# Kernel tuning notes

Measured on AMD Instinct MI355X. Metric: run time of the kernel, lower is better.

The kernel has to match this reference:

```python
import jax, jax.numpy as jnp
import numpy as np

N, E, IN, OUT, R = 50000, 800000, 256, 256, 8
BN_EPS = 1e-5


def setup_inputs() -> dict:
    key = jax.random.key(0)
    ks = jax.random.split(key, 8)
    x = jax.random.normal(ks[0], (N, IN), dtype=jnp.float32)
    edge_index = jax.random.randint(ks[1], (2, E), 0, N, dtype=jnp.int64)
    # edge_attr: 5 float columns; column 4 carries the relation id in [0, R)
    edge_attr = jax.random.randint(ks[2], (E, 5), 0, R).astype(jnp.float32)
    # RGCNConv params (PyG defaults: root_weight=True, bias=True, aggr='mean')
    W = jax.random.normal(ks[3], (R, IN, OUT), dtype=jnp.float32) / np.sqrt(IN)
    root = jax.random.normal(ks[4], (IN, OUT), dtype=jnp.float32) / np.sqrt(IN)
    bias = jnp.zeros((OUT,), dtype=jnp.float32)
    # BatchNorm1d affine params
    gamma = jnp.ones((OUT,), dtype=jnp.float32)
    beta = jnp.zeros((OUT,), dtype=jnp.float32)
    # PReLU single shared slope (torch default init 0.25)
    prelu_a = jnp.asarray(0.25, dtype=jnp.float32)
    return {"x": x, "edge_index": edge_index, "edge_attr": edge_attr,
            "W": W, "root": root, "bias": bias,
            "gamma": gamma, "beta": beta, "prelu_a": prelu_a}


def _rgcn_block(x, edge_index, edge_type, W, root, bias, gamma, beta, prelu_a):
    src, dst = edge_index[0], edge_index[1]
    # per-(relation, dst) mean aggregation via a single segment_sum
    seg = edge_type.astype(jnp.int32) * N + dst.astype(jnp.int32)  # [E]
    msg_sum = jax.ops.segment_sum(x[src], seg, num_segments=R * N)  # [R*N, IN]
    cnt = jax.ops.segment_sum(jnp.ones((E,), x.dtype), seg, num_segments=R * N)
    mean = msg_sum.reshape(R, N, IN) / jnp.maximum(cnt, 1.0).reshape(R, N, 1)
    # relation-specific linear transforms, summed over relations, plus root + bias
    h = jnp.einsum('rni,rio->no', mean, W) + x @ root + bias  # [N, OUT]
    # BatchNorm1d (training mode: batch statistics over nodes)
    mu = jnp.mean(h, axis=0)
    var = jnp.mean(jnp.square(h - mu), axis=0)
    h = (h - mu) * jax.lax.rsqrt(var + BN_EPS) * gamma + beta
    # PReLU (single shared slope); dropout is identity at inference
    h = jnp.where(h > 0, h, prelu_a * h)
    # residual (in_channels == out_channels -> Identity projection)
    return h + x


def reference(x, edge_index, edge_attr, W, root, bias, gamma, beta, prelu_a):
    edge_type = edge_attr[:, 4].astype(jnp.int32)
    return _rgcn_block(x, edge_index, edge_type, W, root, bias, gamma, beta, prelu_a)
```

## Files before the change

kernel.cpp:

```cpp
#include <hip/hip_runtime.h>
#include <cstdio>
#include <cstdint>


constexpr int kN  = 50000;
constexpr int kE  = 800000;
constexpr int kR  = 8;
constexpr int kC  = 256;
constexpr int kMP = 50048;
constexpr int kK  = 2304;
constexpr int kWG = (kMP / 128) * (kC / 128);

typedef __attribute__((ext_vector_type(8))) short bf16x8;
typedef __attribute__((ext_vector_type(4))) float f32x4;
typedef __attribute__((ext_vector_type(2))) unsigned int u32x2;

__device__ __forceinline__ unsigned short f2bf(float f) {
  unsigned u = __builtin_bit_cast(unsigned, f);
  u = u + 0x7FFFu + ((u >> 16) & 1u);
  return (unsigned short)(u >> 16);
}
__device__ __forceinline__ float bf2f(unsigned short s) {
  unsigned u = ((unsigned)s) << 16;
  return __builtin_bit_cast(float, u);
}
__device__ __forceinline__ void gload16(const void* g, void* l) {
  __builtin_amdgcn_global_load_lds((__attribute__((address_space(1))) const void*)g,
                                   (__attribute__((address_space(3))) void*)l, 16, 0, 0);
}

__global__ void k_count(const int* __restrict__ ei, const float* __restrict__ ea,
                        int* __restrict__ cnt) {
  int e = blockIdx.x * blockDim.x + threadIdx.x;
  if (e >= kE) return;
  int dst = ei[kE + e];
  int rel = (int)ea[(size_t)e * 5 + 4];
  if ((unsigned)dst >= (unsigned)kN || (unsigned)rel >= (unsigned)kR) return;
  atomicAdd(&cnt[rel * kN + dst], 1);
}

__global__ void k_convert_x(const float* __restrict__ x, unsigned short* __restrict__ A) {
  int i = (blockIdx.x * blockDim.x + threadIdx.x) * 4;
  if (i >= kN * kC) return;
  int row = i >> 8, col = i & 255;
  float4 v = *(const float4*)(x + i);
  ushort4 o;
  o.x = f2bf(v.x); o.y = f2bf(v.y); o.z = f2bf(v.z); o.w = f2bf(v.w);
  *(ushort4*)(A + (size_t)row * kK + 2048 + col) = o;
}

__global__ void k_convert_w(const float* __restrict__ W, const float* __restrict__ root,
                            unsigned short* __restrict__ wbfT) {
  int t = blockIdx.x * blockDim.x + threadIdx.x;
  if (t >= kC * kK) return;
  int c = t / kK, k = t - c * kK;
  float v;
  if (k < kR * kC) {
    int r = k >> 8, kk = k & 255;
    v = W[(size_t)r * kC * kC + (size_t)kk * kC + c];
  } else {
    v = root[(size_t)(k - kR * kC) * kC + c];
  }
  wbfT[(size_t)c * kK + k] = f2bf(v);
}

__global__ void k_grp(const int* __restrict__ cnt, int* __restrict__ cursor,
                      int* __restrict__ gst, int* __restrict__ cur) {
  int t = blockIdx.x * blockDim.x + threadIdx.x;
  int lane = threadIdx.x & 63;
  int c[kR];
  int gsz = 0;
  if (t < kN) {
#pragma unroll
    for (int r = 0; r < kR; ++r) { c[r] = cnt[r * kN + t]; gsz += c[r]; }
  } else {
#pragma unroll
    for (int r = 0; r < kR; ++r) c[r] = 0;
  }
  int incl = gsz;
#pragma unroll
  for (int d = 1; d < 64; d <<= 1) {
    int v = __shfl_up(incl, d);
    if (lane >= d) incl += v;
  }
  int wtot = __shfl(incl, 63);
  int base = 0;
  if (lane == 63) base = atomicAdd(cursor, wtot);
  base = __shfl(base, 63);
  if (t < kN) {
    int o = base + incl - gsz;
#pragma unroll
    for (int r = 0; r < kR; ++r) { gst[r * kN + t] = o; cur[r * kN + t] = o; o += c[r]; }
  }
}

__global__ void k_fill(const int* __restrict__ ei, const float* __restrict__ ea,
                       int* __restrict__ cur, unsigned short* __restrict__ ebuf) {
  int e = blockIdx.x * blockDim.x + threadIdx.x;
  if (e >= kE) return;
  int src = ei[e];
  int dst = ei[kE + e];
  int rel = (int)ea[(size_t)e * 5 + 4];
  if ((unsigned)dst >= (unsigned)kN || (unsigned)rel >= (unsigned)kR) return;
  int pos = atomicAdd(&cur[rel * kN + dst], 1);
  ebuf[pos] = (unsigned short)src;
}

__global__ __launch_bounds__(256) void k_agg(const unsigned short* __restrict__ ebuf,
                                             const int* __restrict__ gst,
                                             const int* __restrict__ cnt,
                                             unsigned short* A) {
  int w = blockIdx.x * 4 + (threadIdx.x >> 6);
  int lane = threadIdx.x & 63;
  int r = w / kN, dst = w - r * kN;
  int st = gst[w], c = cnt[w];
  const unsigned short* xcols = A + 2048 + lane * 4;
  float s0 = 0.f, s1 = 0.f, s2 = 0.f, s3 = 0.f;
  for (int k = 0; k < c; ++k) {
    int src = ebuf[st + k];
    ushort4 v = *(const ushort4*)(xcols + (size_t)src * kK);
    s0 += bf2f(v.x); s1 += bf2f(v.y); s2 += bf2f(v.z); s3 += bf2f(v.w);
  }
  float sc = c > 0 ? 1.f / (float)c : 0.f;
  unsigned lo = (unsigned)f2bf(s0 * sc) | ((unsigned)f2bf(s1 * sc) << 16);
  unsigned hi = (unsigned)f2bf(s2 * sc) | ((unsigned)f2bf(s3 * sc) << 16);
  u32x2 pk = {lo, hi};
  __builtin_nontemporal_store(pk, (u32x2*)(A + (size_t)dst * kK + r * 256 + lane * 4));
}

__global__ __launch_bounds__(256) void k_gemm(const unsigned short* __restrict__ A,
                                              const unsigned short* __restrict__ wbfT,
                                              float* __restrict__ out,
                                              const float* __restrict__ bias,
                                              float* __restrict__ cs,
                                              float* __restrict__ csq) {
  __shared__ __align__(16) unsigned short As[128 * 64];
  __shared__ __align__(16) unsigned short Bs[128 * 64];
  const int tid = threadIdx.x;
  const int lane = tid & 63, wv = tid >> 6;
  const int bid = blockIdx.x;
  const int xcd = bid & 7, idx = bid >> 3;
  const int wgid = (xcd < 6 ? xcd * 98 : 588 + (xcd - 6) * 97) + idx;
  const int n0 = (wgid & 1) * 128, m0 = (wgid >> 1) * 128;
  const int wm = wv >> 1, wn = wv & 1;
  f32x4 acc[4][4] = {};

  constexpr int NT = kK / 64;
  for (int t = 0; t < NT; ++t) {
    const int kb = t * 64;
#pragma unroll
    for (int i = 0; i < 4; ++i) {
      int l = tid + 256 * i;
      int row = l >> 3;
      int sk = ((l & 7) ^ (row & 7)) * 8;
      gload16(A    + (size_t)(m0 + row) * kK + kb + sk, &As[l * 8]);
      gload16(wbfT + (size_t)(n0 + row) * kK + kb + sk, &Bs[l * 8]);
    }
    asm volatile("s_waitcnt vmcnt(0)" ::: "memory");
    __builtin_amdgcn_s_barrier();
    __builtin_amdgcn_sched_barrier(0);
#pragma unroll
    for (int kk = 0; kk < 64; kk += 32) {
      const int koff = kk + (lane >> 4) * 8;
      bf16x8 a[4], b[4];
#pragma unroll
      for (int i = 0; i < 4; ++i) {
        int ra = wm * 64 + i * 16 + (lane & 15);
        unsigned ba = (unsigned)(koff * 2) ^ (unsigned)((ra & 7) << 4);
        a[i] = *(const bf16x8*)((const char*)As + ra * 128 + ba);
        int rb = wn * 64 + i * 16 + (lane & 15);
        unsigned bb = (unsigned)(koff * 2) ^ (unsigned)((rb & 7) << 4);
        b[i] = *(const bf16x8*)((const char*)Bs + rb * 128 + bb);
      }
#pragma unroll
      for (int i = 0; i < 4; ++i)
#pragma unroll
        for (int j = 0; j < 4; ++j)
          acc[i][j] = __builtin_amdgcn_mfma_f32_16x16x32_bf16(a[i], b[j], acc[i][j], 0, 0, 0);
    }
    __builtin_amdgcn_s_barrier();
    __builtin_amdgcn_sched_barrier(0);
  }

#pragma unroll
  for (int j = 0; j < 4; ++j) {
    int col = n0 + wn * 64 + j * 16 + (lane & 15);
    float bv = bias[col];
    float s = 0.f, ss = 0.f;
#pragma unroll
    for (int i = 0; i < 4; ++i) {
      int rb = m0 + wm * 64 + i * 16 + (lane >> 4) * 4;
#pragma unroll
      for (int q = 0; q < 4; ++q) {
        float v = acc[i][j][q];
        s += v; ss += v * v;
        int row = rb + q;
        if (row < kN) out[(size_t)row * kC + col] = v + bv;
      }
    }
    s  += __shfl_xor(s, 16);  s  += __shfl_xor(s, 32);
    ss += __shfl_xor(ss, 16); ss += __shfl_xor(ss, 32);
    if (lane < 16) { atomicAdd(&cs[col], s); atomicAdd(&csq[col], ss); }
  }
}

__global__ void k_final(float* __restrict__ h, const float* __restrict__ x,
                        const float* __restrict__ cs, const float* __restrict__ csq,
                        const float* __restrict__ bias,
                        const float* __restrict__ gamma, const float* __restrict__ beta,
                        const float* __restrict__ prelu) {
  int idx = (blockIdx.x * blockDim.x + threadIdx.x) * 4;
  if (idx >= kN * kC) return;
  int col = idx & 255;
  const float inv_n = 1.0f / (float)kN;
  float a = prelu[0];
  float4 hv = *(float4*)(h + idx);
  float4 xv = *(const float4*)(x + idx);
  float hr[4] = {hv.x, hv.y, hv.z, hv.w};
  float xr[4] = {xv.x, xv.y, xv.z, xv.w};
#pragma unroll
  for (int j = 0; j < 4; ++j) {
    int c = col + j;
    float mu_raw = cs[c] * inv_n;
    float var = csq[c] * inv_n - mu_raw * mu_raw;
    float mu  = mu_raw + bias[c];
    float k   = gamma[c] * rsqrtf(var + 1e-5f);
    float v   = (hr[j] - mu) * k + beta[c];
    v = v > 0.f ? v : a * v;
    hr[j] = v + xr[j];
  }
  *(float4*)(h + idx) = make_float4(hr[0], hr[1], hr[2], hr[3]);
}

extern "C" void kernel_launch(void* const* d_in, const int* in_sizes, int n_in,
                              void* d_out, int out_size, void* d_ws, size_t ws_size,
                              hipStream_t stream) {
  const float* x     = (const float*)d_in[0];
  const int*   ei    = (const int*)d_in[1];
  const float* ea    = (const float*)d_in[2];
  const float* W     = (const float*)d_in[3];
  const float* root  = (const float*)d_in[4];
  const float* bias  = (const float*)d_in[5];
  const float* gamma = (const float*)d_in[6];
  const float* beta  = (const float*)d_in[7];
  const float* prelu = (const float*)d_in[8];
  float* out = (float*)d_out;
  char* ws = (char*)d_ws;

  size_t o = 0;
  auto alloc = [&](size_t sz) { size_t r = o; o += (sz + 255) & ~(size_t)255; return r; };
  size_t a_o    = alloc((size_t)kMP * kK * 2);
  size_t wbf_o  = alloc((size_t)kC * kK * 2);
  size_t cnt_o  = alloc((size_t)kR * kN * 4);
  size_t cs_o   = alloc(256 * 4);
  size_t csq_o  = alloc(256 * 4);
  size_t csr_o  = alloc(256);
  size_t zend   = o;
  size_t gst_o  = alloc((size_t)kR * kN * 4);
  size_t cur_o  = alloc((size_t)kR * kN * 4);
  size_t eb_o   = alloc((size_t)kE * 2);
  if (o > ws_size) {
    fprintf(stderr, "[RGCN kernel] ws too small: need %zu have %zu\n", o, ws_size);
    return;
  }

  unsigned short* A    = (unsigned short*)(ws + a_o);
  unsigned short* wbfT = (unsigned short*)(ws + wbf_o);
  int*   cnt    = (int*)(ws + cnt_o);
  float* cs     = (float*)(ws + cs_o);
  float* csq    = (float*)(ws + csq_o);
  int*   cursor = (int*)(ws + csr_o);
  int*   gst    = (int*)(ws + gst_o);
  int*   cur    = (int*)(ws + cur_o);
  unsigned short* ebuf = (unsigned short*)(ws + eb_o);

  hipMemsetAsync(ws + cnt_o, 0, zend - cnt_o, stream);
  hipMemsetAsync(ws + a_o + (size_t)kN * kK * 2, 0,
                 (size_t)(kMP - kN) * kK * 2, stream);
  k_count<<<(kE + 255) / 256, 256, 0, stream>>>(ei, ea, cnt);
  k_convert_x<<<(kN * kC / 4) / 256, 256, 0, stream>>>(x, A);
  k_convert_w<<<(kC * kK + 255) / 256, 256, 0, stream>>>(W, root, wbfT);
  k_grp<<<(kN + 255) / 256, 256, 0, stream>>>(cnt, cursor, gst, cur);
  k_fill<<<(kE + 255) / 256, 256, 0, stream>>>(ei, ea, cur, ebuf);
  k_agg<<<(kN * kR) / 4, 256, 0, stream>>>(ebuf, gst, cnt, A);
  k_gemm<<<kWG, 256, 0, stream>>>(A, wbfT, out, bias, cs, csq);
  k_final<<<(kN * kC / 4) / 256, 256, 0, stream>>>(out, x, cs, csq, bias, gamma, beta, prelu);
}
```

Before: 403.1 us.

## Fuse neighbor mean aggregation into GEMM, dropping the materialized A matrix

The separate aggregation kernel, which wrote a 50048x2304 bf16 concat matrix, and the tiled GEMM that re-read it are replaced by one fused kernel. Each 512-thread block gathers per-relation means for 64 destination nodes into LDS, then multiplies them against bf16 weights read directly from global memory, looping over 8 relations plus the root term. k_grp is reorganised so that, within each 64-node chunk, edges of one relation are laid out contiguously. This lets a wave walk one run of edges for 8 destinations at a time. It removes large HBM write and read traffic, but the GEMM now reads B from global or L2 without LDS staging, and the aggregation is serialised per wave inside the block.

```diff
diff --git a/kernel.cpp b/kernel.cpp
--- a/kernel.cpp
+++ b/kernel.cpp
@@ -7,9 +7,8 @@
 constexpr int kE  = 800000;
 constexpr int kR  = 8;
 constexpr int kC  = 256;
-constexpr int kMP = 50048;
 constexpr int kK  = 2304;
-constexpr int kWG = (kMP / 128) * (kC / 128);
+constexpr int kNB = 782;
 
 typedef __attribute__((ext_vector_type(8))) short bf16x8;
 typedef __attribute__((ext_vector_type(4))) float f32x4;
@@ -23,10 +22,6 @@
 __device__ __forceinline__ float bf2f(unsigned short s) {
   unsigned u = ((unsigned)s) << 16;
   return __builtin_bit_cast(float, u);
-}
-__device__ __forceinline__ void gload16(const void* g, void* l) {
-  __builtin_amdgcn_global_load_lds((__attribute__((address_space(1))) const void*)g,
-                                   (__attribute__((address_space(3))) void*)l, 16, 0, 0);
 }
 
 __global__ void k_count(const int* __restrict__ ei, const float* __restrict__ ea,
@@ -39,14 +34,13 @@
   atomicAdd(&cnt[rel * kN + dst], 1);
 }
 
-__global__ void k_convert_x(const float* __restrict__ x, unsigned short* __restrict__ A) {
+__global__ void k_convert_x(const float* __restrict__ x, unsigned short* __restrict__ xbf) {
   int i = (blockIdx.x * blockDim.x + threadIdx.x) * 4;
   if (i >= kN * kC) return;
-  int row = i >> 8, col = i & 255;
   float4 v = *(const float4*)(x + i);
   ushort4 o;
   o.x = f2bf(v.x); o.y = f2bf(v.y); o.z = f2bf(v.z); o.w = f2bf(v.w);
-  *(ushort4*)(A + (size_t)row * kK + 2048 + col) = o;
+  *(ushort4*)(xbf + i) = o;
 }
 
 __global__ void k_convert_w(const float* __restrict__ W, const float* __restrict__ root,
@@ -66,32 +60,23 @@
 
 __global__ void k_grp(const int* __restrict__ cnt, int* __restrict__ cursor,
                       int* __restrict__ gst, int* __restrict__ cur) {
-  int t = blockIdx.x * blockDim.x + threadIdx.x;
+  int wid = (blockIdx.x * blockDim.x + threadIdx.x) >> 6;
   int lane = threadIdx.x & 63;
-  int c[kR];
-  int gsz = 0;
-  if (t < kN) {
-#pragma unroll
-    for (int r = 0; r < kR; ++r) { c[r] = cnt[r * kN + t]; gsz += c[r]; }
-  } else {
-#pragma unroll
-    for (int r = 0; r < kR; ++r) c[r] = 0;
-  }
-  int incl = gsz;
-#pragma unroll
-  for (int d = 1; d < 64; d <<= 1) {
-    int v = __shfl_up(incl, d);
-    if (lane >= d) incl += v;
+  if (wid >= kR * kNB) return;
+  int r = wid / kNB, db = (wid - r * kNB) * 64;
+  int d = db + lane;
+  int c = (d < kN) ? cnt[r * kN + d] : 0;
+  int incl = c;
+#pragma unroll
+  for (int s = 1; s < 64; s <<= 1) {
+    int v = __shfl_up(incl, s);
+    if (lane >= s) incl += v;
   }
   int wtot = __shfl(incl, 63);
   int base = 0;
   if (lane == 63) base = atomicAdd(cursor, wtot);
   base = __shfl(base, 63);
-  if (t < kN) {
-    int o = base + incl - gsz;
-#pragma unroll
-    for (int r = 0; r < kR; ++r) { gst[r * kN + t] = o; cur[r * kN + t] = o; o += c[r]; }
-  }
+  if (d < kN) { int o = base + incl - c; gst[r * kN + d] = o; cur[r * kN + d] = o; }
 }
 
 __global__ void k_fill(const int* __restrict__ ei, const float* __restrict__ ea,
@@ -106,90 +91,133 @@
   ebuf[pos] = (unsigned short)src;
 }
 
-__global__ __launch_bounds__(256) void k_agg(const unsigned short* __restrict__ ebuf,
-                                             const int* __restrict__ gst,
-                                             const int* __restrict__ cnt,
-                                             unsigned short* A) {
-  int w = blockIdx.x * 4 + (threadIdx.x >> 6);
-  int lane = threadIdx.x & 63;
-  int r = w / kN, dst = w - r * kN;
-  int st = gst[w], c = cnt[w];
-  const unsigned short* xcols = A + 2048 + lane * 4;
-  float s0 = 0.f, s1 = 0.f, s2 = 0.f, s3 = 0.f;
-  for (int k = 0; k < c; ++k) {
-    int src = ebuf[st + k];
-    ushort4 v = *(const ushort4*)(xcols + (size_t)src * kK);
-    s0 += bf2f(v.x); s1 += bf2f(v.y); s2 += bf2f(v.z); s3 += bf2f(v.w);
-  }
-  float sc = c > 0 ? 1.f / (float)c : 0.f;
-  unsigned lo = (unsigned)f2bf(s0 * sc) | ((unsigned)f2bf(s1 * sc) << 16);
-  unsigned hi = (unsigned)f2bf(s2 * sc) | ((unsigned)f2bf(s3 * sc) << 16);
-  u32x2 pk = {lo, hi};
-  __builtin_nontemporal_store(pk, (u32x2*)(A + (size_t)dst * kK + r * 256 + lane * 4));
-}
-
-__global__ __launch_bounds__(256) void k_gemm(const unsigned short* __restrict__ A,
-                                              const unsigned short* __restrict__ wbfT,
-                                              float* __restrict__ out,
-                                              const float* __restrict__ bias,
-                                              float* __restrict__ cs,
-                                              float* __restrict__ csq) {
-  __shared__ __align__(16) unsigned short As[128 * 64];
-  __shared__ __align__(16) unsigned short Bs[128 * 64];
-  const int tid = threadIdx.x;
-  const int lane = tid & 63, wv = tid >> 6;
-  const int bid = blockIdx.x;
-  const int xcd = bid & 7, idx = bid >> 3;
-  const int wgid = (xcd < 6 ? xcd * 98 : 588 + (xcd - 6) * 97) + idx;
-  const int n0 = (wgid & 1) * 128, m0 = (wgid >> 1) * 128;
-  const int wm = wv >> 1, wn = wv & 1;
-  f32x4 acc[4][4] = {};
-
-  constexpr int NT = kK / 64;
-  for (int t = 0; t < NT; ++t) {
-    const int kb = t * 64;
-#pragma unroll
-    for (int i = 0; i < 4; ++i) {
-      int l = tid + 256 * i;
-      int row = l >> 3;
-      int sk = ((l & 7) ^ (row & 7)) * 8;
-      gload16(A    + (size_t)(m0 + row) * kK + kb + sk, &As[l * 8]);
-      gload16(wbfT + (size_t)(n0 + row) * kK + kb + sk, &Bs[l * 8]);
+__global__ __launch_bounds__(512) void k_fused(const unsigned short* __restrict__ xbf,
+                                               const unsigned short* __restrict__ wbfT,
+                                               const unsigned short* __restrict__ ebuf,
+                                               const int* __restrict__ gst,
+                                               const int* __restrict__ cnt,
+                                               const float* __restrict__ bias,
+                                               float* __restrict__ out,
+                                               float* __restrict__ cs,
+                                               float* __restrict__ csq) {
+  __shared__ __align__(16) unsigned short Ms[64 * 256];
+  const int tid = threadIdx.x, lane = tid & 63, wv = tid >> 6;
+  const int d0 = blockIdx.x * 64;
+  const int dbase = d0 + wv * 8;
+  f32x4 acc[4][2] = {};
+
+  auto ms_store = [&](int row, float s0, float s1, float s2, float s3) {
+    unsigned lo = (unsigned)f2bf(s0) | ((unsigned)f2bf(s1) << 16);
+    unsigned hi = (unsigned)f2bf(s2) | ((unsigned)f2bf(s3) << 16);
+    unsigned byte = (unsigned)(row * 512) + (((unsigned)(lane * 8)) ^ ((unsigned)((row & 7) << 4)));
+    *(u32x2*)((char*)Ms + byte) = u32x2{lo, hi};
+  };
+
+  for (int r = 0; r < 9; ++r) {
+    if (r < kR) {
+      int vc = kN - dbase; vc = vc < 0 ? 0 : (vc > 8 ? 8 : vc);
+      int gidx = 0;
+      if (vc > 0) {
+        int gb = r * kN + dbase;
+        int myst = 0, myen = 0;
+        if (lane < vc) { myst = gst[gb + lane]; myen = myst + cnt[gb + lane]; }
+        int runSt = __shfl(myst, 0);
+        int runEn = __shfl(myen, vc - 1);
+        int curSt = runSt;
+        int curEn = __shfl(myen, 0);
+        float s0 = 0.f, s1 = 0.f, s2 = 0.f, s3 = 0.f;
+        for (int base = runSt; base < runEn; base += 64) {
+          int p = base + lane;
+          int srcl = (p < runEn) ? (int)ebuf[p] : 0;
+          int nn = runEn - base; if (nn > 64) nn = 64;
+          for (int q = 0; q < nn; q += 4) {
+            int i0 = __shfl(srcl, q);
+            int i1 = __shfl(srcl, (q + 1) & 63);
+            int i2 = __shfl(srcl, (q + 2) & 63);
+            int i3 = __shfl(srcl, (q + 3) & 63);
+            ushort4 v0 = *(const ushort4*)(xbf + (size_t)i0 * kC + lane * 4);
+            ushort4 v1 = *(const ushort4*)(xbf + (size_t)i1 * kC + lane * 4);
+            ushort4 v2 = *(const ushort4*)(xbf + (size_t)i2 * kC + lane * 4);
+            ushort4 v3 = *(const ushort4*)(xbf + (size_t)i3 * kC + lane * 4);
+            ushort4 vv[4] = {v0, v1, v2, v3};
+#pragma unroll
+            for (int i = 0; i < 4; ++i) {
+              if (q + i >= nn) break;
+              int pe = base + q + i;
+              while (pe >= curEn) {
+                int c = curEn - curSt;
+                float sc = c > 0 ? 1.f / (float)c : 0.f;
+                ms_store(wv * 8 + gidx, s0 * sc, s1 * sc, s2 * sc, s3 * sc);
+                s0 = s1 = s2 = s3 = 0.f;
+                ++gidx;
+                curSt = curEn;
+                curEn = __shfl(myen, gidx < vc ? gidx : vc - 1);
+              }
+              s0 += bf2f(vv[i].x); s1 += bf2f(vv[i].y);
+              s2 += bf2f(vv[i].z); s3 += bf2f(vv[i].w);
+            }
+          }
+        }
+        while (gidx < vc) {
+          int c = curEn - curSt;
+          float sc = c > 0 ? 1.f / (float)c : 0.f;
+          ms_store(wv * 8 + gidx, s0 * sc, s1 * sc, s2 * sc, s3 * sc);
+          s0 = s1 = s2 = s3 = 0.f;
+          ++gidx;
+          if (gidx < vc) { curSt = curEn; curEn = __shfl(myen, gidx); }
+        }
+      }
+      for (int g = gidx < 0 ? 0 : (vc > 0 ? vc : 0); g < 8; ++g)
+        ms_store(wv * 8 + g, 0.f, 0.f, 0.f, 0.f);
+    } else {
+      for (int g = 0; g < 8; ++g) {
+        int d = dbase + g;
+        unsigned lo = 0, hi = 0;
+        if (d < kN) {
+          ushort4 v = *(const ushort4*)(xbf + (size_t)d * kC + lane * 4);
+          lo = (unsigned)v.x | ((unsigned)v.y << 16);
+          hi = (unsigned)v.z | ((unsigned)v.w << 16);
+        }
+        int row = wv * 8 + g;
+        unsigned byte = (unsigned)(row * 512) + (((unsigned)(lane * 8)) ^ ((unsigned)((row & 7) << 4)));
+        *(u32x2*)((char*)Ms + byte) = u32x2{lo, hi};
+      }
     }
-    asm volatile("s_waitcnt vmcnt(0)" ::: "memory");
-    __builtin_amdgcn_s_barrier();
-    __builtin_amdgcn_sched_barrier(0);
-#pragma unroll
-    for (int kk = 0; kk < 64; kk += 32) {
+    __syncthreads();
+
+    const int rbase = r * 256;
+#pragma unroll
+    for (int kk = 0; kk < 256; kk += 32) {
       const int koff = kk + (lane >> 4) * 8;
-      bf16x8 a[4], b[4];
+      bf16x8 a[4], b[2];
 #pragma unroll
       for (int i = 0; i < 4; ++i) {
-        int ra = wm * 64 + i * 16 + (lane & 15);
-        unsigned ba = (unsigned)(koff * 2) ^ (unsigned)((ra & 7) << 4);
-        a[i] = *(const bf16x8*)((const char*)As + ra * 128 + ba);
-        int rb = wn * 64 + i * 16 + (lane & 15);
-        unsigned bb = (unsigned)(koff * 2) ^ (unsigned)((rb & 7) << 4);
-        b[i] = *(const bf16x8*)((const char*)Bs + rb * 128 + bb);
+        int row = i * 16 + (lane & 15);
+        unsigned byte = (unsigned)(row * 512) + (((unsigned)(koff * 2)) ^ ((unsigned)((row & 7) << 4)));
+        a[i] = *(const bf16x8*)((const char*)Ms + byte);
+      }
+#pragma unroll
+      for (int j = 0; j < 2; ++j) {
+        int col = wv * 32 + j * 16 + (lane & 15);
+        b[j] = *(const bf16x8*)(wbfT + (size_t)col * kK + rbase + koff);
       }
 #pragma unroll
       for (int i = 0; i < 4; ++i)
 #pragma unroll
-        for (int j = 0; j < 4; ++j)
+        for (int j = 0; j < 2; ++j)
           acc[i][j] = __builtin_amdgcn_mfma_f32_16x16x32_bf16(a[i], b[j], acc[i][j], 0, 0, 0);
     }
-    __builtin_amdgcn_s_barrier();
-    __builtin_amdgcn_sched_barrier(0);
-  }
-
-#pragma unroll
-  for (int j = 0; j < 4; ++j) {
-    int col = n0 + wn * 64 + j * 16 + (lane & 15);
+    __syncthreads();
+  }
+
+#pragma unroll
+  for (int j = 0; j < 2; ++j) {
+    int col = wv * 32 + j * 16 + (lane & 15);
     float bv = bias[col];
     float s = 0.f, ss = 0.f;
 #pragma unroll
     for (int i = 0; i < 4; ++i) {
-      int rb = m0 + wm * 64 + i * 16 + (lane >> 4) * 4;
+      int rb = d0 + i * 16 + (lane >> 4) * 4;
 #pragma unroll
       for (int q = 0; q < 4; ++q) {
         float v = acc[i][j][q];
@@ -249,7 +277,7 @@
 
   size_t o = 0;
   auto alloc = [&](size_t sz) { size_t r = o; o += (sz + 255) & ~(size_t)255; return r; };
-  size_t a_o    = alloc((size_t)kMP * kK * 2);
+  size_t xbf_o  = alloc((size_t)kN * kC * 2);
   size_t wbf_o  = alloc((size_t)kC * kK * 2);
   size_t cnt_o  = alloc((size_t)kR * kN * 4);
   size_t cs_o   = alloc(256 * 4);
@@ -264,7 +292,7 @@
     return;
   }
 
-  unsigned short* A    = (unsigned short*)(ws + a_o);
+  unsigned short* xbf  = (unsigned short*)(ws + xbf_o);
   unsigned short* wbfT = (unsigned short*)(ws + wbf_o);
   int*   cnt    = (int*)(ws + cnt_o);
   float* cs     = (float*)(ws + cs_o);
@@ -275,14 +303,11 @@
   unsigned short* ebuf = (unsigned short*)(ws + eb_o);
 
   hipMemsetAsync(ws + cnt_o, 0, zend - cnt_o, stream);
-  hipMemsetAsync(ws + a_o + (size_t)kN * kK * 2, 0,
-                 (size_t)(kMP - kN) * kK * 2, stream);
   k_count<<<(kE + 255) / 256, 256, 0, stream>>>(ei, ea, cnt);
-  k_convert_x<<<(kN * kC / 4) / 256, 256, 0, stream>>>(x, A);
+  k_convert_x<<<(kN * kC / 4) / 256, 256, 0, stream>>>(x, xbf);
   k_convert_w<<<(kC * kK + 255) / 256, 256, 0, stream>>>(W, root, wbfT);
-  k_grp<<<(kN + 255) / 256, 256, 0, stream>>>(cnt, cursor, gst, cur);
+  k_grp<<<(kR * kNB * 64 + 255) / 256, 256, 0, stream>>>(cnt, cursor, gst, cur);
   k_fill<<<(kE + 255) / 256, 256, 0, stream>>>(ei, ea, cur, ebuf);
-  k_agg<<<(kN * kR) / 4, 256, 0, stream>>>(ebuf, gst, cnt, A);
-  k_gemm<<<kWG, 256, 0, stream>>>(A, wbfT, out, bias, cs, csq);
+  k_fused<<<kNB, 512, 0, stream>>>(xbf, wbfT, ebuf, gst, cnt, bias, out, cs, csq);
   k_final<<<(kN * kC / 4) / 256, 256, 0, stream>>>(out, x, cs, csq, bias, gamma, beta, prelu);
 }
```

Result: slower. 415.0 us (+2.9%).
